# Kernel optimization log

Hardware: AMD Instinct MI355X
Metric: run time of the kernel (lower is better)

## Reference

```python
import jax, jax.numpy as jnp
import numpy as np

N = 100000
E = 1600000
IN_C = 128
HID = 8
HEADS = 8
OUT_C = 40
NEG_SLOPE = 0.2


def _segment_softmax(e, seg, n):
    # e: [E, H], softmax over edges sharing the same destination `seg`
    m = jax.ops.segment_max(e, seg, num_segments=n)
    a = jnp.exp(e - m[seg])
    s = jax.ops.segment_sum(a, seg, num_segments=n)
    return a / (s[seg] + 1e-16)


def _gat_layer(x, src, dst, W, a_src, a_dst, b, heads, concat):
    # PyG GATConv (single-tensor input, shared lin for src/dst), self-loops pre-added.
    n = x.shape[0]
    c = W.shape[0] // heads
    h = (x @ W.T).reshape(n, heads, c)                     # [N, H, C]
    al_s = jnp.einsum('nhc,hc->nh', h, a_src)              # [N, H]
    al_d = jnp.einsum('nhc,hc->nh', h, a_dst)
    e = jax.nn.leaky_relu(al_s[src] + al_d[dst], NEG_SLOPE)  # [E, H]
    alpha = _segment_softmax(e, dst, n)                    # [E, H]
    out = jax.ops.segment_sum(alpha[:, :, None] * h[src], dst, num_segments=n)
    if concat:
        return out.reshape(n, heads * c) + b
    return out.mean(axis=1) + b


def setup_inputs() -> dict:
    key = jax.random.key(0)
    ks = jax.random.split(key, 24)
    HC = HEADS * HID
    def g(k, shape, fan_in):
        return jax.random.normal(k, shape, dtype=jnp.float32) * (1.0 / np.sqrt(fan_in))
    inp = {
        'x': jax.random.normal(ks[0], (N, IN_C), dtype=jnp.float32),
        'edge_index': jax.random.randint(ks[1], (2, E), 0, N, dtype=jnp.int32),
        # layer 0: in -> hidden x heads (concat)
        'W0': g(ks[2], (HC, IN_C), IN_C),
        'as0': g(ks[3], (HEADS, HID), HID),
        'ad0': g(ks[4], (HEADS, HID), HID),
        'b0': jnp.zeros((HC,), jnp.float32),
        'sW0': g(ks[5], (HC, IN_C), IN_C),
        'sb0': jnp.zeros((HC,), jnp.float32),
        # layer 1: HC -> hidden x heads (concat)
        'W1': g(ks[6], (HC, HC), HC),
        'as1': g(ks[7], (HEADS, HID), HID),
        'ad1': g(ks[8], (HEADS, HID), HID),
        'b1': jnp.zeros((HC,), jnp.float32),
        'sW1': g(ks[9], (HC, HC), HC),
        'sb1': jnp.zeros((HC,), jnp.float32),
        # layer 2: HC -> out (concat=False, mean over heads)
        'W2': g(ks[10], (HEADS * OUT_C, HC), HC),
        'as2': g(ks[11], (HEADS, OUT_C), OUT_C),
        'ad2': g(ks[12], (HEADS, OUT_C), OUT_C),
        'b2': jnp.zeros((OUT_C,), jnp.float32),
        'sW2': g(ks[13], (OUT_C, HC), HC),
        'sb2': jnp.zeros((OUT_C,), jnp.float32),
    }
    return inp


def reference(x, edge_index, W0, as0, ad0, b0, sW0, sb0,
              W1, as1, ad1, b1, sW1, sb1,
              W2, as2, ad2, b2, sW2, sb2):
    n = x.shape[0]
    loop = jnp.arange(n, dtype=edge_index.dtype)
    src = jnp.concatenate([edge_index[0], loop])  # add_self_loops=True (PyG default)
    dst = jnp.concatenate([edge_index[1], loop])

    # layer 0
    h = _gat_layer(x, src, dst, W0, as0, ad0, b0, HEADS, True) + (x @ sW0.T + sb0)
    h = jax.nn.elu(h)  # dropout is identity in eval mode
    # layer 1
    h = _gat_layer(h, src, dst, W1, as1, ad1, b1, HEADS, True) + (h @ sW1.T + sb1)
    h = jax.nn.elu(h)
    # layer 2 (concat=False)
    out = _gat_layer(h, src, dst, W2, as2, ad2, b2, HEADS, False) + (h @ sW2.T + sb2)
    return jax.nn.log_softmax(out, axis=-1)
```

## Files before the change

### kernel.cpp

```cpp
#include <hip/hip_runtime.h>
#include <hip/hip_bf16.h>
#include <math.h>

#define HEADS 8
#define NEG_SLOPE 0.2f
#define PBITS 9
#define PBIN 512
#define CHUNK 8192
#define CAP 9216

typedef __attribute__((ext_vector_type(8))) short short8v;
typedef __attribute__((ext_vector_type(4))) float f32x4;

__device__ __forceinline__ float bf2f(unsigned short u) {
    return __uint_as_float(((unsigned int)u) << 16);
}
__device__ __forceinline__ unsigned short f2bf(float f) {
    __hip_bfloat16 h = __float2bfloat16(f);
    union { __hip_bfloat16 h; unsigned short u; } c; c.h = h; return c.u;
}

__global__ __launch_bounds__(256) void k_part(
    const int* __restrict__ ei, int* __restrict__ deg,
    int* __restrict__ binTot, int2* __restrict__ rec, int E) {
    __shared__ int hist[256];
    __shared__ int scanb[256];
    __shared__ int binStart[256];
    __shared__ int cursor[256];
    __shared__ int gbase[256];
    __shared__ int2 stag[CHUNK];
    int tid = threadIdx.x;
    int base = blockIdx.x * CHUNK;

    hist[tid] = 0;
    __syncthreads();
#pragma unroll 1
    for (int k = 0; k < CHUNK / 256; ++k) {
        int i = base + k * 256 + tid;
        if (i < E) {
            int d = ei[E + i];
            atomicAdd(&hist[d >> PBITS], 1);
            atomicAdd(&deg[d], 1);
        }
    }
    __syncthreads();
    int val = hist[tid];
    scanb[tid] = val;
    __syncthreads();
    for (int off = 1; off < 256; off <<= 1) {
        int x = 0;
        if (tid >= off) x = scanb[tid - off];
        __syncthreads();
        scanb[tid] += x;
        __syncthreads();
    }
    int excl = scanb[tid] - val;
    binStart[tid] = excl;
    cursor[tid] = excl;
    if (val > 0) gbase[tid] = atomicAdd(&binTot[tid], val);
    __syncthreads();
    int total = scanb[255];
#pragma unroll 1
    for (int k = 0; k < CHUNK / 256; ++k) {
        int i = base + k * 256 + tid;
        if (i < E) {
            int s = ei[i], d = ei[E + i];
            int pos = atomicAdd(&cursor[d >> PBITS], 1);
            stag[pos] = make_int2(s, d);
        }
    }
    __syncthreads();
#pragma unroll 1
    for (int idx = tid; idx < total; idx += 256) {
        int2 r = stag[idx];
        int b = r.y >> PBITS;
        int gp = gbase[b] + (idx - binStart[b]);
        if (gp < CAP) rec[(size_t)b * CAP + gp] = r;
    }
}

__global__ void k_scan_block(const int* __restrict__ deg, int* __restrict__ offs,
                             int* __restrict__ bsum, int N) {
    __shared__ int lds[256];
    int tid = threadIdx.x;
    int base = blockIdx.x * 1024 + tid * 4;
    int v0 = (base + 0 < N) ? deg[base + 0] + 1 : 0;
    int v1 = (base + 1 < N) ? deg[base + 1] + 1 : 0;
    int v2 = (base + 2 < N) ? deg[base + 2] + 1 : 0;
    int v3 = (base + 3 < N) ? deg[base + 3] + 1 : 0;
    int t01 = v0 + v1;
    int tot = t01 + v2 + v3;
    lds[tid] = tot;
    __syncthreads();
    for (int off = 1; off < 256; off <<= 1) {
        int x = 0;
        if (tid >= off) x = lds[tid - off];
        __syncthreads();
        lds[tid] += x;
        __syncthreads();
    }
    int ex = lds[tid] - tot;
    if (tid == 255) bsum[blockIdx.x] = lds[255];
    if (base + 0 < N) offs[base + 0] = ex;
    if (base + 1 < N) offs[base + 1] = ex + v0;
    if (base + 2 < N) offs[base + 2] = ex + t01;
    if (base + 3 < N) offs[base + 3] = ex + t01 + v2;
}

__global__ void k_scan_top(int* __restrict__ bsum, int nb) {
    __shared__ int lds[256];
    int tid = threadIdx.x;
    int v = (tid < nb) ? bsum[tid] : 0;
    lds[tid] = v;
    __syncthreads();
    for (int off = 1; off < 256; off <<= 1) {
        int x = 0;
        if (tid >= off) x = lds[tid - off];
        __syncthreads();
        lds[tid] += x;
        __syncthreads();
    }
    if (tid < nb) bsum[tid] = lds[tid] - v;
    if (tid == 0) bsum[nb] = lds[255];
}

__global__ void k_scan_add(int* __restrict__ offs, const int* __restrict__ bsum, int N) {
    int i = blockIdx.x * 256 + threadIdx.x;
    if (i < N) offs[i] += bsum[i >> 10];
    if (i == 0) offs[N] = bsum[(N + 1023) >> 10];
}

__global__ __launch_bounds__(256) void k_build(
    const int2* __restrict__ rec, const int* __restrict__ binTot,
    const int* __restrict__ offs, int* __restrict__ csr, int N) {
    __shared__ int loff[PBIN];
    __shared__ int lcnt[PBIN];
    int b = blockIdx.x;
    int tid = threadIdx.x;
    int n0 = b << PBITS;
    for (int q = tid; q < PBIN; q += 256) {
        lcnt[q] = 0;
        int n = n0 + q;
        if (n < N) {
            int o = offs[n];
            loff[q] = o;
            csr[o] = n;
        }
    }
    __syncthreads();
    int cnt = min(binTot[b], CAP);
    const int2* basep = rec + (size_t)b * CAP;
#pragma unroll 1
    for (int i = tid; i < cnt; i += 256) {
        int2 r = basep[i];
        int l = r.y & (PBIN - 1);
        int rank = atomicAdd(&lcnt[l], 1);
        csr[loff[l] + 1 + rank] = r.x;
    }
}

template <int CPT, int M1, int M2, bool AL_FOLD, bool A_BF16>
__global__ __launch_bounds__(256) void k_gemm_dual(
    const float* __restrict__ X, const float* __restrict__ Wa, const float* __restrict__ Wb,
    const float* __restrict__ bias1, const float* __restrict__ bias2,
    void* __restrict__ outa_, float* __restrict__ outb,
    const float* __restrict__ as_w, const float* __restrict__ ad_w, float* __restrict__ AL,
    int N, int K) {
    constexpr int M = M1 + M2;
    static_assert(CPT * 16 >= M, "CPT too small");
    __shared__ float sW[CPT * 16][68];
    __shared__ float sX[64][68];
    int tx = threadIdx.x, ty = threadIdx.y;
    int tid = ty * 16 + tx;
    int r0 = blockIdx.x * 64;

    float acc[4][CPT];
#pragma unroll
    for (int jc = 0; jc < CPT; ++jc) {
        int col = tx + 16 * jc;
        float b = 0.f;
        if (col >= M1 && col < M) b = bias1[col - M1] + bias2[col - M1];
#pragma unroll
        for (int jr = 0; jr < 4; ++jr) acc[jr][jc] = b;
    }

    for (int k0 = 0; k0 < K; k0 += 64) {
        __syncthreads();
        for (int idx = tid; idx < CPT * 16 * 16; idx += 256) {
            int c = idx >> 4, kq = (idx & 15) * 4;
            float4 v = make_float4(0.f, 0.f, 0.f, 0.f);
            if (c < M1) v = *(const float4*)&Wa[(size_t)c * K + k0 + kq];
            else if (c < M) v = *(const float4*)&Wb[(size_t)(c - M1) * K + k0 + kq];
            *(float4*)&sW[c][kq] = v;
        }
        for (int idx = tid; idx < 64 * 16; idx += 256) {
            int r = idx >> 4, kq = (idx & 15) * 4;
            int gr = r0 + r;
            float4 v = make_float4(0.f, 0.f, 0.f, 0.f);
            if (gr < N) v = *(const float4*)&X[(size_t)gr * K + k0 + kq];
            *(float4*)&sX[r][kq] = v;
        }
        __syncthreads();

        for (int k = 0; k < 64; k += 4) {
            float4 xr[4];
#pragma unroll
            for (int jr = 0; jr < 4; ++jr) xr[jr] = *(const float4*)&sX[ty * 4 + jr][k];
#pragma unroll
            for (int jc = 0; jc < CPT; ++jc) {
                float4 wc = *(const float4*)&sW[tx + 16 * jc][k];
#pragma unroll
                for (int jr = 0; jr < 4; ++jr)
                    acc[jr][jc] += wc.x * xr[jr].x + wc.y * xr[jr].y +
                                   wc.z * xr[jr].z + wc.w * xr[jr].w;
            }
        }
    }

#pragma unroll
    for (int jr = 0; jr < 4; ++jr) {
        int gr = r0 + ty * 4 + jr;
        if (gr >= N) continue;
#pragma unroll
        for (int jc = 0; jc < CPT; ++jc) {
            int col = tx + 16 * jc;
            if (col < M1) {
                if (A_BF16) ((unsigned short*)outa_)[(size_t)gr * M1 + col] = f2bf(acc[jr][jc]);
                else        ((float*)outa_)[(size_t)gr * M1 + col] = acc[jr][jc];
            } else if (col < M) {
                outb[(size_t)gr * M2 + (col - M1)] = acc[jr][jc];
            }
        }
    }

    if constexpr (AL_FOLD) {
        __syncthreads();
        float* sH = &sW[0][0];
#pragma unroll
        for (int jr = 0; jr < 4; ++jr)
#pragma unroll
            for (int jc = 0; jc < 4; ++jc)
                sH[(ty * 4 + jr) * 68 + (tx + 16 * jc)] = acc[jr][jc];
        __syncthreads();
        int j = tid & 15, hd = j & 7;
        const float* a = (j < 8 ? as_w : ad_w) + hd * 8;
        float av[8];
#pragma unroll
        for (int c = 0; c < 8; ++c) av[c] = a[c];
#pragma unroll
        for (int q = 0; q < 4; ++q) {
            int row = (tid >> 4) + 16 * q;
            int gr = r0 + row;
            if (gr < N) {
                float sum = 0.f;
#pragma unroll
                for (int c = 0; c < 8; ++c) sum += av[c] * sH[row * 68 + hd * 8 + c];
                AL[(size_t)gr * 16 + j] = sum;
            }
        }
    }
}

__global__ void k_prep2(const float* __restrict__ W2, const float* __restrict__ as2,
                        const float* __restrict__ ad2, float* __restrict__ wt,
                        __hip_bfloat16* __restrict__ w2sw) {
    if (blockIdx.x < 96) {
        int t = blockIdx.x * 256 + threadIdx.x;
        int j = t & 7;
        int rc = t >> 3;
        int col = rc % 48, c = rc / 48;
        int k = c * 8 + j;
        int hd = k >> 6, kk = k & 63;
        float v = (col < 40) ? W2[(size_t)(hd * 40 + col) * 64 + kk] : 0.f;
        w2sw[t] = __float2bfloat16(v);
    } else {
        for (int t = threadIdx.x; t < 1024; t += 256) {
            int j = t >> 6, k = t & 63;
            int hd = j & 7;
            const float* a = (j < 8 ? as2 : ad2) + hd * 40;
            float sum = 0.f;
            for (int c = 0; c < 40; ++c) sum += a[c] * W2[(size_t)(hd * 40 + c) * 64 + k];
            wt[j * 64 + k] = sum;
        }
    }
}

__global__ __launch_bounds__(256, 8) void k_fused(
    const unsigned short* __restrict__ Hb, const float* __restrict__ AL,
    const int* __restrict__ offs, const int* __restrict__ csr,
    float* __restrict__ S, unsigned short* __restrict__ Sb, int N) {
    int wid = threadIdx.x >> 6, lane = threadIdx.x & 63;
    int n = blockIdx.x * 4 + wid;
    if (n >= N) return;
    int off = offs[n], deg = offs[n + 1] - off;
    int el = lane >> 3, hd = lane & 7;
    int dp = lane & 31, es = lane >> 5;
    int hp = dp >> 2;
    float ald = AL[(size_t)n * 16 + 8 + hd];

    int src_c = 0; float e_c = 0.f;
    if (el < deg) {
        src_c = csr[off + el];
        float t = AL[(size_t)src_c * 16 + hd] + ald;
        e_c = __expf(t > 0.f ? t : NEG_SLOPE * t);
    }

    float s_run = 0.f, ax = 0.f, ay = 0.f;
    for (int b0 = 0; b0 < deg; b0 += 8) {
        unsigned int hv[4];
#pragma unroll
        for (int j = 0; j < 4; ++j) {
            int sj = __shfl(src_c, (2 * j + es) * 8);
            hv[j] = *(const unsigned int*)&Hb[(size_t)sj * 64 + 2 * dp];
        }
        int en = b0 + 8 + el;
        int src_n = 0; float e_n = 0.f;
        if (en < deg) {
            src_n = csr[off + en];
            float t = AL[(size_t)src_n * 16 + hd] + ald;
            e_n = __expf(t > 0.f ? t : NEG_SLOPE * t);
        }

        s_run += e_c;
#pragma unroll
        for (int j = 0; j < 4; ++j) {
            float a = __shfl(e_c, (2 * j + es) * 8 + hp);
            unsigned int u = hv[j];
            ax += a * bf2f((unsigned short)(u & 0xffff));
            ay += a * bf2f((unsigned short)(u >> 16));
        }
        src_c = src_n; e_c = e_n;
    }
#pragma unroll
    for (int d = 8; d <= 32; d <<= 1) s_run += __shfl_xor(s_run, d);
    float sf = __shfl(s_run, hp);
    float inv = 1.0f / (sf + 1e-16f);
    ax *= inv; ay *= inv;
    ax += __shfl_xor(ax, 32);
    ay += __shfl_xor(ay, 32);
    if (es == 0) {
        float2 sk = *(const float2*)&S[(size_t)n * 64 + 2 * dp];
        float vx = sk.x + ax, vy = sk.y + ay;
        vx = vx > 0.f ? vx : expm1f(vx);
        vy = vy > 0.f ? vy : expm1f(vy);
        *(float2*)&S[(size_t)n * 64 + 2 * dp] = make_float2(vx, vy);
        if (Sb) {
            ushort2 w;
            w.x = f2bf(vx); w.y = f2bf(vy);
            *(ushort2*)&Sb[(size_t)n * 64 + 2 * dp] = w;
        }
    }
}

__global__ __launch_bounds__(256, 8) void k_l2f(
    const unsigned short* __restrict__ Xb, const float* __restrict__ AL,
    const float* __restrict__ SK, const __hip_bfloat16* __restrict__ w2sw,
    const int* __restrict__ offs, const int* __restrict__ csr,
    float* __restrict__ out, int N) {
    __shared__ __hip_bfloat16 sA[64 * 16 * 8];
    __shared__ float sC[16][48];
    __shared__ float sW8[4][64];
    int wid = threadIdx.x >> 6, lane = threadIdx.x & 63;
    int el = lane >> 3, hd = lane & 7;
    int dp = lane & 31, eh = lane >> 5;

#pragma unroll 1
    for (int p = 0; p < 4; ++p) {
        int mrow = wid * 4 + p;
        int n = blockIdx.x * 16 + mrow;
        float2 acc[4];
#pragma unroll
        for (int h2 = 0; h2 < 4; ++h2) acc[h2] = make_float2(0.f, 0.f);
        if (n < N) {
            int off = offs[n], deg = offs[n + 1] - off;
            float ald = AL[(size_t)n * 16 + 8 + hd];

            int src_c = 0; float e_c = 0.f;
            if (el < deg) {
                src_c = csr[off + el];
                float t = AL[(size_t)src_c * 16 + hd] + ald;
                e_c = __expf(t > 0.f ? t : NEG_SLOPE * t);
            }

            float s_run = 0.f;
#pragma unroll 1
            for (int b0 = 0; b0 < deg; b0 += 8) {
                unsigned int xv0[4];
#pragma unroll
                for (int j = 0; j < 4; ++j) {
                    int sj = __shfl(src_c, j * 8);
                    xv0[j] = *(const unsigned int*)&Xb[(size_t)sj * 64 + 2 * dp];
                }
                int en = b0 + 8 + el;
                int src_n = 0; float e_n = 0.f;
                if (en < deg) {
                    src_n = csr[off + en];
                    float t = AL[(size_t)src_n * 16 + hd] + ald;
                    e_n = __expf(t > 0.f ? t : NEG_SLOPE * t);
                }

                sW8[wid][lane] = e_c;
                s_run += e_c;
#pragma unroll
                for (int j = 0; j < 4; ++j) {
                    float4 a4 = *(const float4*)&sW8[wid][j * 8 + 4 * eh];
                    float hx = bf2f((unsigned short)(xv0[j] & 0xffff));
                    float hy = bf2f((unsigned short)(xv0[j] >> 16));
                    acc[0].x += a4.x * hx; acc[0].y += a4.x * hy;
                    acc[1].x += a4.y * hx; acc[1].y += a4.y * hy;
                    acc[2].x += a4.z * hx; acc[2].y += a4.z * hy;
                    acc[3].x += a4.w * hx; acc[3].y += a4.w * hy;
                }
#pragma unroll
                for (int j = 0; j < 4; ++j) {
                    int sj = __shfl(src_c, (j + 4) * 8);
                    xv0[j] = *(const unsigned int*)&Xb[(size_t)sj * 64 + 2 * dp];
                }
#pragma unroll
                for (int j = 0; j < 4; ++j) {
                    float4 a4 = *(const float4*)&sW8[wid][(j + 4) * 8 + 4 * eh];
                    float hx = bf2f((unsigned short)(xv0[j] & 0xffff));
                    float hy = bf2f((unsigned short)(xv0[j] >> 16));
                    acc[0].x += a4.x * hx; acc[0].y += a4.x * hy;
                    acc[1].x += a4.y * hx; acc[1].y += a4.y * hy;
                    acc[2].x += a4.z * hx; acc[2].y += a4.z * hy;
                    acc[3].x += a4.w * hx; acc[3].y += a4.w * hy;
                }
                src_c = src_n; e_c = e_n;
            }
#pragma unroll
            for (int d = 8; d <= 32; d <<= 1) s_run += __shfl_xor(s_run, d);
#pragma unroll
            for (int h2 = 0; h2 < 4; ++h2) {
                float sv = __shfl(s_run, 4 * eh + h2);
                float iv = 1.0f / (sv + 1e-16f);
                acc[h2].x *= iv; acc[h2].y *= iv;
            }
        }
#pragma unroll
        for (int h2 = 0; h2 < 4; ++h2) {
            int K0 = (4 * eh + h2) * 64 + 2 * dp;
            int chunk = K0 >> 3, pos = K0 & 7;
            ushort2 w;
            w.x = f2bf(acc[h2].x); w.y = f2bf(acc[h2].y);
            *(ushort2*)&sA[chunk * 128 + ((mrow + chunk) & 15) * 8 + pos] = w;
        }
    }
    __syncthreads();

    if (wid < 3) {
        f32x4 cacc = {0.f, 0.f, 0.f, 0.f};
        int grp = lane >> 4;
        int r16 = lane & 15;
#pragma unroll 4
        for (int ks = 0; ks < 16; ++ks) {
            int c = ks * 4 + grp;
            short8v av = *(const short8v*)&sA[c * 128 + ((r16 + c) & 15) * 8];
            short8v bv = *(const short8v*)&w2sw[(size_t)(c * 48 + wid * 16 + r16) * 8];
            cacc = __builtin_amdgcn_mfma_f32_16x16x32_bf16(av, bv, cacc, 0, 0, 0);
        }
#pragma unroll
        for (int jj = 0; jj < 4; ++jj)
            sC[grp * 4 + jj][wid * 16 + r16] = cacc[jj];
    }
    __syncthreads();

    for (int p = 0; p < 4; ++p) {
        int mrow = wid * 4 + p;
        int n = blockIdx.x * 16 + mrow;
        if (n >= N) continue;
        float val = (lane < 40) ? SK[(size_t)n * 40 + lane] + sC[mrow][lane] * 0.125f : -INFINITY;
        float mx = val;
#pragma unroll
        for (int d = 32; d; d >>= 1) mx = fmaxf(mx, __shfl_xor(mx, d));
        float ex = (lane < 40) ? __expf(val - mx) : 0.f;
        float sm = ex;
#pragma unroll
        for (int d = 32; d; d >>= 1) sm += __shfl_xor(sm, d);
        if (lane < 40) out[(size_t)n * 40 + lane] = val - mx - logf(sm);
    }
}

extern "C" void kernel_launch(void* const* d_in, const int* in_sizes, int n_in,
                              void* d_out, int out_size, void* d_ws, size_t ws_size,
                              hipStream_t stream) {
    const float* x   = (const float*)d_in[0];
    const int*   ei  = (const int*)d_in[1];
    const float* W0  = (const float*)d_in[2];
    const float* as0 = (const float*)d_in[3];
    const float* ad0 = (const float*)d_in[4];
    const float* b0  = (const float*)d_in[5];
    const float* sW0 = (const float*)d_in[6];
    const float* sb0 = (const float*)d_in[7];
    const float* W1  = (const float*)d_in[8];
    const float* as1 = (const float*)d_in[9];
    const float* ad1 = (const float*)d_in[10];
    const float* b1  = (const float*)d_in[11];
    const float* sW1 = (const float*)d_in[12];
    const float* sb1 = (const float*)d_in[13];
    const float* W2  = (const float*)d_in[14];
    const float* as2 = (const float*)d_in[15];
    const float* ad2 = (const float*)d_in[16];
    const float* b2  = (const float*)d_in[17];
    const float* sW2 = (const float*)d_in[18];
    const float* sb2 = (const float*)d_in[19];
    float* out = (float*)d_out;

    int N = in_sizes[0] / 128;
    int E = in_sizes[1] / 2;
    int NBIN = (N + PBIN - 1) >> PBITS;

    char* wsp = (char*)d_ws;
    size_t woff = 0;
    auto A = [&](size_t nbytes) -> void* {
        void* p = wsp + woff;
        woff = (woff + nbytes + 255) & ~(size_t)255;
        return p;
    };
    int* offs   = (int*)A((size_t)(N + 1) * 4);
    int* deg    = (int*)A((size_t)N * 4);
    int* bsum   = (int*)A(4096);
    int* binTot = (int*)A((size_t)(NBIN + 1) * 4);
    int* csr    = (int*)A((size_t)(E + N) * 4);
    int2* rec   = (int2*)A((size_t)NBIN * CAP * 8);
    float* wt   = (float*)A(1024 * 4);
    __hip_bfloat16* w2sw = (__hip_bfloat16*)A(64 * 48 * 8 * 2);
    float* AL   = (float*)A((size_t)N * 16 * 4);
    float* S    = (float*)A((size_t)N * 64 * 4);
    float* T    = (float*)A((size_t)N * 64 * 4);
    unsigned short* Hb = (unsigned short*)A((size_t)N * 64 * 2);
    unsigned short* Tb = (unsigned short*)A((size_t)N * 64 * 2);
    (void)ws_size; (void)n_in; (void)out_size;

    hipMemsetAsync(deg, 0, (size_t)N * 4, stream);
    hipMemsetAsync(binTot, 0, (size_t)(NBIN + 1) * 4, stream);
    int gPart = (E + CHUNK - 1) / CHUNK;
    k_part<<<gPart, 256, 0, stream>>>(ei, deg, binTot, rec, E);
    int nb = (N + 1023) / 1024;
    k_scan_block<<<nb, 256, 0, stream>>>(deg, offs, bsum, N);
    k_scan_top<<<1, 256, 0, stream>>>(bsum, nb);
    k_scan_add<<<(N + 255) / 256, 256, 0, stream>>>(offs, bsum, N);
    k_build<<<NBIN, 256, 0, stream>>>(rec, binTot, offs, csr, N);

    k_prep2<<<97, 256, 0, stream>>>(W2, as2, ad2, wt, w2sw);

    dim3 bG(16, 16);
    int gG = (N + 63) / 64;
    int gN4 = (N + 3) / 4;

    k_gemm_dual<8, 64, 64, true, true><<<gG, bG, 0, stream>>>(
        x, W0, sW0, b0, sb0, Hb, S, as0, ad0, AL, N, 128);
    k_fused<<<gN4, 256, 0, stream>>>(Hb, AL, offs, csr, S, nullptr, N);

    k_gemm_dual<8, 64, 64, true, true><<<gG, bG, 0, stream>>>(
        S, W1, sW1, b1, sb1, Hb, T, as1, ad1, AL, N, 64);
    k_fused<<<gN4, 256, 0, stream>>>(Hb, AL, offs, csr, T, Tb, N);

    k_gemm_dual<4, 16, 40, false, false><<<gG, bG, 0, stream>>>(
        T, wt, sW2, b2, sb2, AL, S, nullptr, nullptr, nullptr, N, 64);
    k_l2f<<<(N + 15) / 16, 256, 0, stream>>>(Tb, AL, S, w2sw, offs, csr, out, N);
}
```

Before: 486.0 us.

## Store attention logits in bf16 and use packed FMA in layer-2 aggregation

```diff
diff --git a/kernel.cpp b/kernel.cpp
--- a/kernel.cpp
+++ b/kernel.cpp
@@ -164,8 +164,8 @@
     const float* __restrict__ X, const float* __restrict__ Wa, const float* __restrict__ Wb,
     const float* __restrict__ bias1, const float* __restrict__ bias2,
     void* __restrict__ outa_, float* __restrict__ outb,
-    const float* __restrict__ as_w, const float* __restrict__ ad_w, float* __restrict__ AL,
-    int N, int K) {
+    const float* __restrict__ as_w, const float* __restrict__ ad_w,
+    unsigned short* __restrict__ AL, int N, int K) {
     constexpr int M = M1 + M2;
     static_assert(CPT * 16 >= M, "CPT too small");
     __shared__ float sW[CPT * 16][68];
@@ -255,7 +255,7 @@
                 float sum = 0.f;
 #pragma unroll
                 for (int c = 0; c < 8; ++c) sum += av[c] * sH[row * 68 + hd * 8 + c];
-                AL[(size_t)gr * 16 + j] = sum;
+                AL[(size_t)gr * 16 + j] = f2bf(sum);
             }
         }
     }
@@ -286,7 +286,7 @@
 }
 
 __global__ __launch_bounds__(256, 8) void k_fused(
-    const unsigned short* __restrict__ Hb, const float* __restrict__ AL,
+    const unsigned short* __restrict__ Hb, const unsigned short* __restrict__ AL,
     const int* __restrict__ offs, const int* __restrict__ csr,
     float* __restrict__ S, unsigned short* __restrict__ Sb, int N) {
     int wid = threadIdx.x >> 6, lane = threadIdx.x & 63;
@@ -296,12 +296,12 @@
     int el = lane >> 3, hd = lane & 7;
     int dp = lane & 31, es = lane >> 5;
     int hp = dp >> 2;
-    float ald = AL[(size_t)n * 16 + 8 + hd];
+    float ald = bf2f(AL[(size_t)n * 16 + 8 + hd]);
 
     int src_c = 0; float e_c = 0.f;
     if (el < deg) {
         src_c = csr[off + el];
-        float t = AL[(size_t)src_c * 16 + hd] + ald;
+        float t = bf2f(AL[(size_t)src_c * 16 + hd]) + ald;
         e_c = __expf(t > 0.f ? t : NEG_SLOPE * t);
     }
 
@@ -317,7 +317,7 @@
         int src_n = 0; float e_n = 0.f;
         if (en < deg) {
             src_n = csr[off + en];
-            float t = AL[(size_t)src_n * 16 + hd] + ald;
+            float t = bf2f(AL[(size_t)src_n * 16 + hd]) + ald;
             e_n = __expf(t > 0.f ? t : NEG_SLOPE * t);
         }
 
@@ -353,7 +353,7 @@
 }
 
 __global__ __launch_bounds__(256, 8) void k_l2f(
-    const unsigned short* __restrict__ Xb, const float* __restrict__ AL,
+    const unsigned short* __restrict__ Xb, const unsigned short* __restrict__ AL,
     const float* __restrict__ SK, const __hip_bfloat16* __restrict__ w2sw,
     const int* __restrict__ offs, const int* __restrict__ csr,
     float* __restrict__ out, int N) {
@@ -368,21 +368,21 @@
     for (int p = 0; p < 4; ++p) {
         int mrow = wid * 4 + p;
         int n = blockIdx.x * 16 + mrow;
-        float2 acc[4];
-#pragma unroll
-        for (int h2 = 0; h2 < 4; ++h2) acc[h2] = make_float2(0.f, 0.f);
-        if (n < N) {
+        float2 acc0 = make_float2(0.f, 0.f), acc1 = make_float2(0.f, 0.f);
+        float2 acc2 = make_float2(0.f, 0.f), acc3 = make_float2(0.f, 0.f);
+        float s_run = 0.f;
+        bool live = (n < N);
+        if (live) {
             int off = offs[n], deg = offs[n + 1] - off;
-            float ald = AL[(size_t)n * 16 + 8 + hd];
+            float ald = bf2f(AL[(size_t)n * 16 + 8 + hd]);
 
             int src_c = 0; float e_c = 0.f;
             if (el < deg) {
                 src_c = csr[off + el];
-                float t = AL[(size_t)src_c * 16 + hd] + ald;
+                float t = bf2f(AL[(size_t)src_c * 16 + hd]) + ald;
                 e_c = __expf(t > 0.f ? t : NEG_SLOPE * t);
             }
 
-            float s_run = 0.f;
 #pragma unroll 1
             for (int b0 = 0; b0 < deg; b0 += 8) {
                 unsigned int xv0[4];
@@ -395,7 +395,7 @@
                 int src_n = 0; float e_n = 0.f;
                 if (en < deg) {
                     src_n = csr[off + en];
-                    float t = AL[(size_t)src_n * 16 + hd] + ald;
+                    float t = bf2f(AL[(size_t)src_n * 16 + hd]) + ald;
                     e_n = __expf(t > 0.f ? t : NEG_SLOPE * t);
                 }
 
@@ -404,12 +404,19 @@
 #pragma unroll
                 for (int j = 0; j < 4; ++j) {
                     float4 a4 = *(const float4*)&sW8[wid][j * 8 + 4 * eh];
-                    float hx = bf2f((unsigned short)(xv0[j] & 0xffff));
-                    float hy = bf2f((unsigned short)(xv0[j] >> 16));
-                    acc[0].x += a4.x * hx; acc[0].y += a4.x * hy;
-                    acc[1].x += a4.y * hx; acc[1].y += a4.y * hy;
-                    acc[2].x += a4.z * hx; acc[2].y += a4.z * hy;
-                    acc[3].x += a4.w * hx; acc[3].y += a4.w * hy;
+                    float2 alo = make_float2(a4.x, a4.y);
+                    float2 ahi = make_float2(a4.z, a4.w);
+                    unsigned int u = xv0[j];
+                    float2 x2 = make_float2(__uint_as_float(u << 16),
+                                            __uint_as_float(u & 0xffff0000u));
+                    asm("v_pk_fma_f32 %0, %1, %2, %0 op_sel:[0,0,0] op_sel_hi:[0,1,1]"
+                        : "+v"(acc0) : "v"(alo), "v"(x2));
+                    asm("v_pk_fma_f32 %0, %1, %2, %0 op_sel:[1,0,0] op_sel_hi:[1,1,1]"
+                        : "+v"(acc1) : "v"(alo), "v"(x2));
+                    asm("v_pk_fma_f32 %0, %1, %2, %0 op_sel:[0,0,0] op_sel_hi:[0,1,1]"
+                        : "+v"(acc2) : "v"(ahi), "v"(x2));
+                    asm("v_pk_fma_f32 %0, %1, %2, %0 op_sel:[1,0,0] op_sel_hi:[1,1,1]"
+                        : "+v"(acc3) : "v"(ahi), "v"(x2));
                 }
 #pragma unroll
                 for (int j = 0; j < 4; ++j) {
@@ -419,30 +426,40 @@
 #pragma unroll
                 for (int j = 0; j < 4; ++j) {
                     float4 a4 = *(const float4*)&sW8[wid][(j + 4) * 8 + 4 * eh];
-                    float hx = bf2f((unsigned short)(xv0[j] & 0xffff));
-                    float hy = bf2f((unsigned short)(xv0[j] >> 16));
-                    acc[0].x += a4.x * hx; acc[0].y += a4.x * hy;
-                    acc[1].x += a4.y * hx; acc[1].y += a4.y * hy;
-                    acc[2].x += a4.z * hx; acc[2].y += a4.z * hy;
-                    acc[3].x += a4.w * hx; acc[3].y += a4.w * hy;
+                    float2 alo = make_float2(a4.x, a4.y);
+                    float2 ahi = make_float2(a4.z, a4.w);
+                    unsigned int u = xv0[j];
+                    float2 x2 = make_float2(__uint_as_float(u << 16),
+                                            __uint_as_float(u & 0xffff0000u));
+                    asm("v_pk_fma_f32 %0, %1, %2, %0 op_sel:[0,0,0] op_sel_hi:[0,1,1]"
+                        : "+v"(acc0) : "v"(alo), "v"(x2));
+                    asm("v_pk_fma_f32 %0, %1, %2, %0 op_sel:[1,0,0] op_sel_hi:[1,1,1]"
+                        : "+v"(acc1) : "v"(alo), "v"(x2));
+                    asm("v_pk_fma_f32 %0, %1, %2, %0 op_sel:[0,0,0] op_sel_hi:[0,1,1]"
+                        : "+v"(acc2) : "v"(ahi), "v"(x2));
+                    asm("v_pk_fma_f32 %0, %1, %2, %0 op_sel:[1,0,0] op_sel_hi:[1,1,1]"
+                        : "+v"(acc3) : "v"(ahi), "v"(x2));
                 }
                 src_c = src_n; e_c = e_n;
             }
 #pragma unroll
             for (int d = 8; d <= 32; d <<= 1) s_run += __shfl_xor(s_run, d);
-#pragma unroll
-            for (int h2 = 0; h2 < 4; ++h2) {
-                float sv = __shfl(s_run, 4 * eh + h2);
-                float iv = 1.0f / (sv + 1e-16f);
-                acc[h2].x *= iv; acc[h2].y *= iv;
-            }
-        }
+            float sv0 = __shfl(s_run, 4 * eh + 0); float iv0 = 1.0f / (sv0 + 1e-16f);
+            float sv1 = __shfl(s_run, 4 * eh + 1); float iv1 = 1.0f / (sv1 + 1e-16f);
+            float sv2 = __shfl(s_run, 4 * eh + 2); float iv2 = 1.0f / (sv2 + 1e-16f);
+            float sv3 = __shfl(s_run, 4 * eh + 3); float iv3 = 1.0f / (sv3 + 1e-16f);
+            acc0.x *= iv0; acc0.y *= iv0;
+            acc1.x *= iv1; acc1.y *= iv1;
+            acc2.x *= iv2; acc2.y *= iv2;
+            acc3.x *= iv3; acc3.y *= iv3;
+        }
+        float2 av[4] = {acc0, acc1, acc2, acc3};
 #pragma unroll
         for (int h2 = 0; h2 < 4; ++h2) {
             int K0 = (4 * eh + h2) * 64 + 2 * dp;
             int chunk = K0 >> 3, pos = K0 & 7;
             ushort2 w;
-            w.x = f2bf(acc[h2].x); w.y = f2bf(acc[h2].y);
+            w.x = f2bf(av[h2].x); w.y = f2bf(av[h2].y);
             *(ushort2*)&sA[chunk * 128 + ((mrow + chunk) & 15) * 8 + pos] = w;
         }
     }
@@ -455,9 +472,9 @@
 #pragma unroll 4
         for (int ks = 0; ks < 16; ++ks) {
             int c = ks * 4 + grp;
-            short8v av = *(const short8v*)&sA[c * 128 + ((r16 + c) & 15) * 8];
+            short8v avv = *(const short8v*)&sA[c * 128 + ((r16 + c) & 15) * 8];
             short8v bv = *(const short8v*)&w2sw[(size_t)(c * 48 + wid * 16 + r16) * 8];
-            cacc = __builtin_amdgcn_mfma_f32_16x16x32_bf16(av, bv, cacc, 0, 0, 0);
+            cacc = __builtin_amdgcn_mfma_f32_16x16x32_bf16(avv, bv, cacc, 0, 0, 0);
         }
 #pragma unroll
         for (int jj = 0; jj < 4; ++jj)
@@ -525,7 +542,7 @@
     int2* rec   = (int2*)A((size_t)NBIN * CAP * 8);
     float* wt   = (float*)A(1024 * 4);
     __hip_bfloat16* w2sw = (__hip_bfloat16*)A(64 * 48 * 8 * 2);
-    float* AL   = (float*)A((size_t)N * 16 * 4);
+    unsigned short* AL = (unsigned short*)A((size_t)N * 16 * 2);
     float* S    = (float*)A((size_t)N * 64 * 4);
     float* T    = (float*)A((size_t)N * 64 * 4);
     unsigned short* Hb = (unsigned short*)A((size_t)N * 64 * 2);
@@ -556,7 +573,7 @@
         S, W1, sW1, b1, sb1, Hb, T, as1, ad1, AL, N, 64);
     k_fused<<<gN4, 256, 0, stream>>>(Hb, AL, offs, csr, T, Tb, N);
 
-    k_gemm_dual<4, 16, 40, false, false><<<gG, bG, 0, stream>>>(
+    k_gemm_dual<4, 16, 40, false, true><<<gG, bG, 0, stream>>>(
         T, wt, sW2, b2, sb2, AL, S, nullptr, nullptr, nullptr, N, 64);
     k_l2f<<<(N + 15) / 16, 256, 0, stream>>>(Tb, AL, S, w2sw, offs, csr, out, N);
 }
```

Result: no change. 484.2 us (-0.4%).
